# Optimization experiments

Measured on AMD Instinct MI355X. Metric: run time of the kernel, lower is better.

## Reference

```python
import jax, jax.numpy as jnp
import numpy as np
import math

D_IN = 1024
D_OUT = 1024
NUM_HEADS = 16
HEAD_DIM = D_OUT // NUM_HEADS
B = 2
S = 4096


def setup_inputs() -> dict:
    key = jax.random.key(0)
    ks = jax.random.split(key, 6)
    x = jax.random.normal(ks[0], (B, S, D_IN), dtype=jnp.float32)
    # kaiming-uniform-ish scale for weights; exact init values don't matter for correctness
    bound = 1.0 / math.sqrt(D_IN)
    Wq = jax.random.uniform(ks[1], (D_OUT, D_IN), minval=-bound, maxval=bound, dtype=jnp.float32)
    Wk = jax.random.uniform(ks[2], (D_OUT, D_IN), minval=-bound, maxval=bound, dtype=jnp.float32)
    Wv = jax.random.uniform(ks[3], (D_OUT, D_IN), minval=-bound, maxval=bound, dtype=jnp.float32)
    Wo = jax.random.uniform(ks[4], (D_OUT, D_OUT), minval=-bound, maxval=bound, dtype=jnp.float32)
    bo = jax.random.uniform(ks[5], (D_OUT,), minval=-bound, maxval=bound, dtype=jnp.float32)
    return {"x": x, "Wq": Wq, "Wk": Wk, "Wv": Wv, "Wo": Wo, "bo": bo}


@jax.custom_vjp
def binarize(w):
    return jnp.sign(w)

def _bin_fwd(w):
    return jnp.sign(w), w

def _bin_bwd(w, g):
    # straight-through estimator: pass grad where |w| <= 1
    return (g * (jnp.abs(w) <= 1).astype(g.dtype),)

binarize.defvjp(_bin_fwd, _bin_bwd)


def reference(x, Wq, Wk, Wv, Wo, bo):
    b, n, _ = x.shape
    h, hd = NUM_HEADS, HEAD_DIM
    # binarized projections (torch F.linear: x @ W.T)
    q = (x @ binarize(Wq).T).reshape(b, n, h, hd).transpose(0, 2, 1, 3)  # [b,h,n,hd]
    k = (x @ binarize(Wk).T).reshape(b, n, h, hd).transpose(0, 2, 1, 3)
    v = (x @ binarize(Wv).T).reshape(b, n, h, hd).transpose(0, 2, 1, 3)
    scores = jnp.einsum('bhqd,bhkd->bhqk', q, k) / math.sqrt(hd)  # [b,h,n,n]
    causal = jnp.tril(jnp.ones((n, n), dtype=bool))
    scores = jnp.where(causal, scores, -jnp.inf)
    attn = jax.nn.softmax(scores, axis=-1)
    # dropout p=0.0 -> identity
    ctx = jnp.einsum('bhqk,bhkd->bqhd', attn, v).reshape(b, n, h * hd)
    return ctx @ binarize(Wo).T + bo
```

## Files before the change

### kernel.cpp

```cpp
#include <hip/hip_runtime.h>
#include <hip/hip_bf16.h>
#include <cstdint>
#include <cstddef>

#define S 4096
#define D 1024
#define H 16
#define HD 64
#define BATCH 2
#define M_TOK 8192
#define K2 2048

typedef short short8 __attribute__((ext_vector_type(8)));
typedef __bf16 bf16x8 __attribute__((ext_vector_type(8)));
typedef float f32x4 __attribute__((ext_vector_type(4)));
typedef float f32x16 __attribute__((ext_vector_type(16)));
typedef unsigned int u32;

static __device__ __forceinline__ ushort f2bf(float f) {
  union { float f; uint32_t u; } v; v.f = f;
  uint32_t u = v.u + 0x7FFFu + ((v.u >> 16) & 1u);
  return (ushort)(u >> 16);
}
static __device__ __forceinline__ float bf2f(ushort h) {
  union { uint32_t u; float f; } v; v.u = ((uint32_t)h) << 16; return v.f;
}
static __device__ __forceinline__ uint32_t cvtpk(float lo, float hi) {
  uint32_t r;
  asm("v_cvt_pk_bf16_f32 %0, %1, %2" : "=v"(r) : "v"(lo), "v"(hi));
  return r;
}
static __device__ __forceinline__ float vexp2(float x) {
  float r;
  asm("v_exp_f32 %0, %1" : "=v"(r) : "v"(x));
  return r;
}
static __device__ __forceinline__ bf16x8 pack4(uint32_t a, uint32_t b, uint32_t c, uint32_t d) {
  union { uint32_t u[4]; bf16x8 v; } z;
  z.u[0] = a; z.u[1] = b; z.u[2] = c; z.u[3] = d;
  return z.v;
}
static __device__ __forceinline__ void gld16(const void* g, void* l) {
  __builtin_amdgcn_global_load_lds(
      (const __attribute__((address_space(1))) u32*)g,
      (__attribute__((address_space(3))) u32*)l, 16, 0, 0);
}
static __device__ __forceinline__ ushort sgn(float a) {
  return a > 0.f ? 0x3F80 : (a < 0.f ? 0xBF80 : 0);
}

__global__ void prep_x(const float* __restrict__ x, ushort* __restrict__ xcat) {
  int i = blockIdx.x * blockDim.x + threadIdx.x;
  const int total = M_TOK * 128;
  for (; i < total; i += gridDim.x * blockDim.x) {
    int row = i >> 7, c8 = (i & 127) * 8;
    const float* px = &x[(size_t)row * 1024 + c8];
    float4 a = *(const float4*)px;
    float4 b = *(const float4*)(px + 4);
    float va[8] = {a.x, a.y, a.z, a.w, b.x, b.y, b.z, b.w};
    union { ushort u[8]; short8 v; } Hh, Ll;
#pragma unroll
    for (int j = 0; j < 8; ++j) {
      ushort h = f2bf(va[j]);
      Hh.u[j] = h;
      Ll.u[j] = f2bf(va[j] - bf2f(h));
    }
    *(short8*)&xcat[(size_t)row * K2 + c8] = Hh.v;
    *(short8*)&xcat[(size_t)row * K2 + 1024 + c8] = Ll.v;
  }
}

__global__ void prep_w(const float* __restrict__ wq, const float* __restrict__ wk,
                       const float* __restrict__ wv, const float* __restrict__ wo,
                       ushort* __restrict__ wcat, ushort* __restrict__ wob) {
  int i = blockIdx.x * blockDim.x + threadIdx.x;
  const int total = (D * D) / 4;
  for (; i < total; i += gridDim.x * blockDim.x) {
    float4 a;
    union { ushort u[4]; uint2 v; } t;
    a = *(const float4*)&wq[i * 4];
    t.u[0] = sgn(a.x); t.u[1] = sgn(a.y); t.u[2] = sgn(a.z); t.u[3] = sgn(a.w);
    *(uint2*)&wcat[i * 4] = t.v;
    a = *(const float4*)&wk[i * 4];
    t.u[0] = sgn(a.x); t.u[1] = sgn(a.y); t.u[2] = sgn(a.z); t.u[3] = sgn(a.w);
    *(uint2*)&wcat[D * D + i * 4] = t.v;
    a = *(const float4*)&wv[i * 4];
    t.u[0] = sgn(a.x); t.u[1] = sgn(a.y); t.u[2] = sgn(a.z); t.u[3] = sgn(a.w);
    *(uint2*)&wcat[2 * D * D + i * 4] = t.v;
    a = *(const float4*)&wo[i * 4];
    t.u[0] = sgn(a.x); t.u[1] = sgn(a.y); t.u[2] = sgn(a.z); t.u[3] = sgn(a.w);
    *(uint2*)&wob[i * 4] = t.v;
  }
}

__global__ __launch_bounds__(512, 2) void gemm256(
    const ushort* __restrict__ A, const ushort* __restrict__ Bw,
    ushort* __restrict__ q_hi, ushort* __restrict__ q_lo,
    ushort* __restrict__ k_hi, ushort* __restrict__ k_lo)
{
  __shared__ ushort smA[3][256 * 32];
  __shared__ ushort smB[3][256 * 32];
  const int tid = threadIdx.x;
  const int l = tid & 63;
  const int w = tid >> 6;
  const int x = l & 15, g = l >> 4;
  const int wm = w >> 2, wn = w & 3;
  const int bm = blockIdx.x, bn = blockIdx.y;

  const ushort* gA[2]; const ushort* gB[2]; int ldso[2];
#pragma unroll
  for (int r = 0; r < 2; ++r) {
    int q = r * 512 + tid;
    int row = q >> 2;
    int blk = (q & 3) ^ ((row & 3) ^ ((row >> 2) & 3));
    gA[r] = &A[(size_t)(bm * 256 + row) * 2048 + blk * 8];
    gB[r] = &Bw[(size_t)(bn * 256 + row) * 1024 + blk * 8];
    ldso[r] = (r * 512 + w * 64) * 8;
  }

  f32x4 acc[8][4] = {};

#pragma unroll
  for (int r = 0; r < 2; ++r) {
    gld16(gA[r] + 0, &smA[0][ldso[r]]);
    gld16(gB[r] + 0, &smB[0][ldso[r]]);
  }
#pragma unroll
  for (int r = 0; r < 2; ++r) {
    gld16(gA[r] + 32, &smA[1][ldso[r]]);
    gld16(gB[r] + ((32) & 1023), &smB[1][ldso[r]]);
  }

  const int swz = (x & 3) ^ ((x >> 2) & 3);
  int cb = 0;
  for (int s = 0; s < 64; ++s) {
    if (s < 63) {
      asm volatile("s_waitcnt vmcnt(4)" ::: "memory");
    } else {
      asm volatile("s_waitcnt vmcnt(0)" ::: "memory");
    }
    __builtin_amdgcn_s_barrier();

    if (s + 2 < 64) {
      int nb = cb - 1; if (nb < 0) nb = 2;
      int k0 = (s + 2) * 32;
#pragma unroll
      for (int r = 0; r < 2; ++r) {
        gld16(gA[r] + k0, &smA[nb][ldso[r]]);
        gld16(gB[r] + (k0 & 1023), &smB[nb][ldso[r]]);
      }
    }

    const ushort* bA = smA[cb];
    const ushort* bB = smB[cb];
    bf16x8 af[8], bf_[4];
#pragma unroll
    for (int m = 0; m < 8; ++m)
      af[m] = *(const bf16x8*)&bA[(wm * 128 + m * 16 + x) * 32 + (g ^ swz) * 8];
#pragma unroll
    for (int n = 0; n < 4; ++n)
      bf_[n] = *(const bf16x8*)&bB[(wn * 64 + n * 16 + x) * 32 + (g ^ swz) * 8];

    __builtin_amdgcn_s_setprio(1);
#pragma unroll
    for (int m = 0; m < 8; ++m)
#pragma unroll
      for (int n = 0; n < 4; ++n)
        acc[m][n] = __builtin_amdgcn_mfma_f32_16x16x32_bf16(af[m], bf_[n], acc[m][n], 0, 0, 0);
    __builtin_amdgcn_s_setprio(0);

    cb = (cb == 2) ? 0 : cb + 1;
  }

#pragma unroll
  for (int m = 0; m < 8; ++m)
#pragma unroll
    for (int n = 0; n < 4; ++n)
#pragma unroll
      for (int r = 0; r < 4; ++r) {
        int rowg = bm * 256 + wm * 128 + m * 16 + g * 4 + r;
        int colg = bn * 256 + wn * 64 + n * 16 + x;
        float v = acc[m][n][r];
        int bi = rowg >> 12, ntok = rowg & 4095;
        int proj = colg >> 10;
        int cg = colg & 1023;
        int h = cg >> 6, hd = cg & 63;
        ushort* oh = (proj == 0) ? q_hi : k_hi;
        ushort* ol = (proj == 0) ? q_lo : k_lo;
        size_t off = (size_t)(bi * H + h) * (S * HD) + (size_t)ntok * HD + hd;
        ushort hiv = f2bf(v);
        oh[off] = hiv;
        ol[off] = f2bf(v - bf2f(hiv));
      }
}

template<int EPI, int KK, int BROW, int AST>
__global__ __launch_bounds__(256) void gemm97(
    const ushort* __restrict__ A, const ushort* __restrict__ Bw,
    ushort* __restrict__ v_t,
    float* __restrict__ of, const float* __restrict__ bias)
{
  __shared__ ushort smA[128 * 32];
  __shared__ ushort smB[128 * 32];
  const int tid = threadIdx.x;
  const int l = tid & 63;
  const int w = tid >> 6;
  const int x = l & 15, g = l >> 4;
  const int wm = w >> 1, wn = w & 1;
  const int bm = blockIdx.x, bn = blockIdx.y;

  const ushort* gA[2]; const ushort* gB[2]; int ldso[2];
#pragma unroll
  for (int p = 0; p < 2; ++p) {
    int q = p * 256 + tid;
    gA[p] = &A[(size_t)(bm * 128 + (q >> 2)) * AST + (q & 3) * 8];
    gB[p] = &Bw[(size_t)(bn * 128 + (q >> 2)) * BROW + (q & 3) * 8];
    ldso[p] = (p * 256 + w * 64) * 8;
  }

  f32x4 acc[4][4] = {};

  for (int k0 = 0; k0 < KK; k0 += 32) {
    __syncthreads();
#pragma unroll
    for (int p = 0; p < 2; ++p) {
      gld16(gA[p] + k0, &smA[ldso[p]]);
      gld16(gB[p] + (k0 & (BROW - 1)), &smB[ldso[p]]);
    }
    __syncthreads();
    bf16x8 af[4], bf_[4];
#pragma unroll
    for (int m = 0; m < 4; ++m)
      af[m] = *(const bf16x8*)&smA[(wm * 64 + m * 16 + x) * 32 + g * 8];
#pragma unroll
    for (int n = 0; n < 4; ++n)
      bf_[n] = *(const bf16x8*)&smB[(wn * 64 + n * 16 + x) * 32 + g * 8];
#pragma unroll
    for (int m = 0; m < 4; ++m)
#pragma unroll
      for (int n = 0; n < 4; ++n)
        acc[m][n] = __builtin_amdgcn_mfma_f32_16x16x32_bf16(af[m], bf_[n], acc[m][n], 0, 0, 0);
  }

#pragma unroll
  for (int m = 0; m < 4; ++m)
#pragma unroll
    for (int n = 0; n < 4; ++n)
#pragma unroll
      for (int r = 0; r < 4; ++r) {
        int rowg = bm * 128 + wm * 64 + m * 16 + g * 4 + r;
        int colg = bn * 128 + wn * 64 + n * 16 + x;
        float v = acc[m][n][r];
        if (EPI == 2) {
          of[(size_t)rowg * D + colg] = v + bias[colg];
        } else {
          int bi = rowg >> 12, ntok = rowg & 4095;
          int cg = colg & 1023;
          int h = cg >> 6, hd = cg & 63;
          size_t bhb = (size_t)(bi * H + h) * (S * HD);
          v_t[bhb + (size_t)hd * S + ntok] = f2bf(v);
        }
      }
}

__global__ __launch_bounds__(256) void flash16(
    const ushort* __restrict__ qhi, const ushort* __restrict__ qlo,
    const ushort* __restrict__ khi, const ushort* __restrict__ klo,
    const ushort* __restrict__ vt, ushort* __restrict__ ctx)
{
  __shared__ ushort smKhi[2][64 * 64];
  __shared__ ushort smKlo[2][64 * 64];
  __shared__ ushort smVT[2][64 * 64];

  const int tid = threadIdx.x;
  const int l = tid & 63;
  const int w = tid >> 6;
  const int q31 = l & 31;
  const int g2 = l >> 5;
  const int l7 = l & 7;
  const int bh = blockIdx.x;
  const int qt = (int)(gridDim.y - 1) - (int)blockIdx.y;
  const int qbase = qt * 128;
  const size_t qkbase = (size_t)bh * S * HD;

  int soff_k[2]; size_t soff_v[2]; int ldso[2];
#pragma unroll
  for (int p = 0; p < 2; ++p) {
    int q = p * 256 + tid;
    int r2 = q >> 3;
    int sb = (q & 7) ^ (r2 & 7);
    soff_k[p] = r2 * HD + sb * 8;
    soff_v[p] = (size_t)r2 * S + sb * 8;
    ldso[p] = (p * 256 + w * 64) * 8;
  }
  const ushort* khb = khi + qkbase;
  const ushort* klb = klo + qkbase;
  const ushort* vtb = vt + qkbase;

  bf16x8 bq[2][4];
  {
    int qrow = qbase + w * 32 + q31;
    size_t base = qkbase + (size_t)qrow * HD + g2 * 8;
#pragma unroll
    for (int s2 = 0; s2 < 4; ++s2) {
      bq[0][s2] = *(const bf16x8*)&qhi[base + s2 * 16];
      bq[1][s2] = *(const bf16x8*)&qlo[base + s2 * 16];
    }
  }

  float mrun = -1e30f;
  float lrun = 0.f;
  f32x16 oacc0 = {}, oacc1 = {};

  const int kvmax = (qbase + 127) >> 6;
  const int qmaxw = qbase + w * 32 + 31;
  const float C1 = 0.125f * 1.44269504f;
  const float TH = 8.0f / C1;

#pragma unroll
  for (int p = 0; p < 2; ++p) {
    gld16(khb + soff_k[p], &smKhi[0][ldso[p]]);
    gld16(klb + soff_k[p], &smKlo[0][ldso[p]]);
    gld16(vtb + soff_v[p], &smVT[0][ldso[p]]);
  }
  __syncthreads();

  int cur = 0;
  for (int kv = 0; kv <= kvmax; ++kv) {
    if (kv < kvmax) {
      const ushort* kh = khb + (size_t)(kv + 1) * (64 * HD);
      const ushort* kl = klb + (size_t)(kv + 1) * (64 * HD);
      const ushort* vp = vtb + (size_t)(kv + 1) * 64;
      int nb = cur ^ 1;
#pragma unroll
      for (int p = 0; p < 2; ++p) {
        gld16(kh + soff_k[p], &smKhi[nb][ldso[p]]);
        gld16(kl + soff_k[p], &smKlo[nb][ldso[p]]);
        gld16(vp + soff_v[p], &smVT[nb][ldso[p]]);
      }
    }

    if (kv * 64 <= qmaxw) {
      const ushort* bKhi = smKhi[cur];
      const ushort* bKlo = smKlo[cur];
      const ushort* bVT = smVT[cur];

      f32x16 sc0 = {}, sc1 = {};
      __builtin_amdgcn_s_setprio(1);
#pragma unroll
      for (int s2 = 0; s2 < 4; ++s2) {
        {
          int row = q31;
          int pb = row * 64 + (((2 * s2 + g2)) ^ l7) * 8;
          bf16x8 kH = *(const bf16x8*)&bKhi[pb];
          bf16x8 kL = *(const bf16x8*)&bKlo[pb];
          sc0 = __builtin_amdgcn_mfma_f32_32x32x16_bf16(kH, bq[0][s2], sc0, 0, 0, 0);
          sc0 = __builtin_amdgcn_mfma_f32_32x32x16_bf16(kL, bq[0][s2], sc0, 0, 0, 0);
          sc0 = __builtin_amdgcn_mfma_f32_32x32x16_bf16(kH, bq[1][s2], sc0, 0, 0, 0);
        }
        {
          int row = 32 + q31;
          int pb = row * 64 + (((2 * s2 + g2)) ^ l7) * 8;
          bf16x8 kH = *(const bf16x8*)&bKhi[pb];
          bf16x8 kL = *(const bf16x8*)&bKlo[pb];
          sc1 = __builtin_amdgcn_mfma_f32_32x32x16_bf16(kH, bq[0][s2], sc1, 0, 0, 0);
          sc1 = __builtin_amdgcn_mfma_f32_32x32x16_bf16(kL, bq[0][s2], sc1, 0, 0, 0);
          sc1 = __builtin_amdgcn_mfma_f32_32x32x16_bf16(kH, bq[1][s2], sc1, 0, 0, 0);
        }
      }
      __builtin_amdgcn_s_setprio(0);

      if (kv * 64 + 63 > qbase + w * 32) {
        int qglob = qbase + w * 32 + q31;
        int kb = kv * 64 + 4 * g2;
#pragma unroll
        for (int r = 0; r < 16; ++r) {
          int k5 = (r & 3) + 8 * (r >> 2);
          if (kb + k5 > qglob) sc0[r] = -1e30f;
          if (kb + 32 + k5 > qglob) sc1[r] = -1e30f;
        }
      }

      float mt[8];
#pragma unroll
      for (int r = 0; r < 8; ++r)
        mt[r] = fmaxf(fmaxf(sc0[2 * r], sc0[2 * r + 1]), fmaxf(sc1[2 * r], sc1[2 * r + 1]));
      float mloc = fmaxf(fmaxf(fmaxf(mt[0], mt[1]), fmaxf(mt[2], mt[3])),
                         fmaxf(fmaxf(mt[4], mt[5]), fmaxf(mt[6], mt[7])));
      if (__any(mloc > mrun + TH)) {
        float mx = fmaxf(mloc, __shfl_xor(mloc, 32));
        float mnew = fmaxf(mrun, mx);
        float scal = vexp2((mrun - mnew) * C1);
        mrun = mnew;
        lrun *= scal;
        oacc0 *= scal;
        oacc1 *= scal;
      }
      float mc = mrun * C1;
#pragma unroll
      for (int r = 0; r < 16; ++r) {
        sc0[r] = vexp2(sc0[r] * C1 - mc);
        sc1[r] = vexp2(sc1[r] * C1 - mc);
      }
      float st[8];
#pragma unroll
      for (int r = 0; r < 8; ++r)
        st[r] = (sc0[2 * r] + sc0[2 * r + 1]) + (sc1[2 * r] + sc1[2 * r + 1]);
      lrun += ((st[0] + st[1]) + (st[2] + st[3])) + ((st[4] + st[5]) + (st[6] + st[7]));

      uint32_t pbw[4][4];
#pragma unroll
      for (int s2 = 0; s2 < 4; ++s2) {
        const int s1 = s2 & 1;
#pragma unroll
        for (int p = 0; p < 2; ++p) {
          uint32_t a, b;
          if (s2 < 2) {
            a = cvtpk(sc0[2 * p + 8 * s1], sc0[2 * p + 1 + 8 * s1]);
            b = cvtpk(sc0[2 * p + 4 + 8 * s1], sc0[2 * p + 5 + 8 * s1]);
          } else {
            a = cvtpk(sc1[2 * p + 8 * s1], sc1[2 * p + 1 + 8 * s1]);
            b = cvtpk(sc1[2 * p + 4 + 8 * s1], sc1[2 * p + 5 + 8 * s1]);
          }
          asm volatile("v_permlane32_swap_b32 %0, %1" : "+v"(a), "+v"(b));
          pbw[s2][p] = a;
          pbw[s2][2 + p] = b;
        }
      }

      __builtin_amdgcn_s_setprio(1);
#pragma unroll
      for (int s2 = 0; s2 < 4; ++s2) {
        bf16x8 bp = pack4(pbw[s2][0], pbw[s2][1], pbw[s2][2], pbw[s2][3]);
        {
          bf16x8 vf = *(const bf16x8*)&bVT[(q31)*64 + (((2 * s2 + g2)) ^ l7) * 8];
          oacc0 = __builtin_amdgcn_mfma_f32_32x32x16_bf16(vf, bp, oacc0, 0, 0, 0);
        }
        {
          bf16x8 vf = *(const bf16x8*)&bVT[(32 + q31) * 64 + (((2 * s2 + g2)) ^ l7) * 8];
          oacc1 = __builtin_amdgcn_mfma_f32_32x32x16_bf16(vf, bp, oacc1, 0, 0, 0);
        }
      }
      __builtin_amdgcn_s_setprio(0);
    }

    __syncthreads();
    cur ^= 1;
  }

  const int b = bh >> 4, h = bh & 15;
  {
    float ls = lrun + __shfl_xor(lrun, 32);
    float inv = 1.0f / ls;
    int tok = qbase + w * 32 + q31;
    size_t rbase = (size_t)(b * S + tok) * D + h * 64;
#pragma unroll
    for (int r2 = 0; r2 < 4; ++r2) {
      uint2 uu;
      uu.x = cvtpk(oacc0[4 * r2] * inv, oacc0[4 * r2 + 1] * inv);
      uu.y = cvtpk(oacc0[4 * r2 + 2] * inv, oacc0[4 * r2 + 3] * inv);
      *(uint2*)&ctx[rbase + 8 * r2 + 4 * g2] = uu;
      uu.x = cvtpk(oacc1[4 * r2] * inv, oacc1[4 * r2 + 1] * inv);
      uu.y = cvtpk(oacc1[4 * r2 + 2] * inv, oacc1[4 * r2 + 3] * inv);
      *(uint2*)&ctx[rbase + 32 + 8 * r2 + 4 * g2] = uu;
    }
  }
}

extern "C" void kernel_launch(void* const* d_in, const int* in_sizes, int n_in,
                              void* d_out, int out_size, void* d_ws, size_t ws_size,
                              hipStream_t stream) {
  const float* x  = (const float*)d_in[0];
  const float* Wq = (const float*)d_in[1];
  const float* Wk = (const float*)d_in[2];
  const float* Wv = (const float*)d_in[3];
  const float* Wo = (const float*)d_in[4];
  const float* bo = (const float*)d_in[5];
  float* out = (float*)d_out;

  if (ws_size < (size_t)120 * 1024 * 1024) return;

  char* ws = (char*)d_ws;
  const size_t MB = 1024 * 1024;
  ushort* xcat = (ushort*)(ws);
  ushort* ctx  = (ushort*)(ws);
  ushort* wcat = (ushort*)(ws + 32 * MB);
  ushort* wob  = (ushort*)(ws + 38 * MB);
  ushort* qhi  = (ushort*)(ws + 40 * MB);
  ushort* qlo  = (ushort*)(ws + 56 * MB);
  ushort* khi  = (ushort*)(ws + 72 * MB);
  ushort* klo  = (ushort*)(ws + 88 * MB);
  ushort* vt   = (ushort*)(ws + 104 * MB);

  prep_x<<<2048, 256, 0, stream>>>(x, xcat);
  prep_w<<<1024, 256, 0, stream>>>(Wq, Wk, Wv, Wo, wcat, wob);

  gemm256<<<dim3(32, 8), 512, 0, stream>>>(xcat, wcat, qhi, qlo, khi, klo);
  gemm97<1, 1024, 1024, 2048><<<dim3(64, 8), 256, 0, stream>>>(
      xcat, wcat + 2 * D * D, vt, nullptr, nullptr);

  flash16<<<dim3(BATCH * H, S / 128), 256, 0, stream>>>(qhi, qlo, khi, klo, vt, ctx);

  gemm97<2, 1024, 1024, 1024><<<dim3(64, 8), 256, 0, stream>>>(
      ctx, wob, nullptr, out, bo);
}
```

Before: 321.0 us.

## Fold V projection into the QK projection GEMM launch with variable K-loop length

The V projection GEMM, previously its own launch, now runs as four extra column-tile groups of the big 256x256 QK GEMM grid. Those blocks run a shorter K loop (32 steps over the hi part only) and write bf16 V transposed. This removes one kernel launch and fills the device with more blocks in a single wave schedule. In exchange the grid becomes load-imbalanced because V blocks finish in half the time, and the epilogue now carries a branch.

```diff
diff --git a/kernel.cpp b/kernel.cpp
--- a/kernel.cpp
+++ b/kernel.cpp
@@ -96,7 +96,8 @@
 __global__ __launch_bounds__(512, 2) void gemm256(
     const ushort* __restrict__ A, const ushort* __restrict__ Bw,
     ushort* __restrict__ q_hi, ushort* __restrict__ q_lo,
-    ushort* __restrict__ k_hi, ushort* __restrict__ k_lo)
+    ushort* __restrict__ k_hi, ushort* __restrict__ k_lo,
+    ushort* __restrict__ v_t)
 {
   __shared__ ushort smA[3][256 * 32];
   __shared__ ushort smB[3][256 * 32];
@@ -106,6 +107,7 @@
   const int x = l & 15, g = l >> 4;
   const int wm = w >> 2, wn = w & 3;
   const int bm = blockIdx.x, bn = blockIdx.y;
+  const int NS = (bn < 8) ? 64 : 32;
 
   const ushort* gA[2]; const ushort* gB[2]; int ldso[2];
 #pragma unroll
@@ -133,15 +135,15 @@
 
   const int swz = (x & 3) ^ ((x >> 2) & 3);
   int cb = 0;
-  for (int s = 0; s < 64; ++s) {
-    if (s < 63) {
+  for (int s = 0; s < NS; ++s) {
+    if (s < NS - 1) {
       asm volatile("s_waitcnt vmcnt(4)" ::: "memory");
     } else {
       asm volatile("s_waitcnt vmcnt(0)" ::: "memory");
     }
     __builtin_amdgcn_s_barrier();
 
-    if (s + 2 < 64) {
+    if (s + 2 < NS) {
       int nb = cb - 1; if (nb < 0) nb = 2;
       int k0 = (s + 2) * 32;
 #pragma unroll
@@ -182,22 +184,26 @@
         int colg = bn * 256 + wn * 64 + n * 16 + x;
         float v = acc[m][n][r];
         int bi = rowg >> 12, ntok = rowg & 4095;
-        int proj = colg >> 10;
         int cg = colg & 1023;
         int h = cg >> 6, hd = cg & 63;
-        ushort* oh = (proj == 0) ? q_hi : k_hi;
-        ushort* ol = (proj == 0) ? q_lo : k_lo;
-        size_t off = (size_t)(bi * H + h) * (S * HD) + (size_t)ntok * HD + hd;
-        ushort hiv = f2bf(v);
-        oh[off] = hiv;
-        ol[off] = f2bf(v - bf2f(hiv));
-      }
-}
-
-template<int EPI, int KK, int BROW, int AST>
-__global__ __launch_bounds__(256) void gemm97(
+        size_t bhb = (size_t)(bi * H + h) * (S * HD);
+        if (bn < 8) {
+          int proj = colg >> 10;
+          ushort* oh = (proj == 0) ? q_hi : k_hi;
+          ushort* ol = (proj == 0) ? q_lo : k_lo;
+          size_t off = bhb + (size_t)ntok * HD + hd;
+          ushort hiv = f2bf(v);
+          oh[off] = hiv;
+          ol[off] = f2bf(v - bf2f(hiv));
+        } else {
+          v_t[bhb + (size_t)hd * S + ntok] = f2bf(v);
+        }
+      }
+}
+
+template<int KK, int BROW, int AST>
+__global__ __launch_bounds__(256) void gemm97o(
     const ushort* __restrict__ A, const ushort* __restrict__ Bw,
-    ushort* __restrict__ v_t,
     float* __restrict__ of, const float* __restrict__ bias)
 {
   __shared__ ushort smA[128 * 32];
@@ -250,16 +256,7 @@
       for (int r = 0; r < 4; ++r) {
         int rowg = bm * 128 + wm * 64 + m * 16 + g * 4 + r;
         int colg = bn * 128 + wn * 64 + n * 16 + x;
-        float v = acc[m][n][r];
-        if (EPI == 2) {
-          of[(size_t)rowg * D + colg] = v + bias[colg];
-        } else {
-          int bi = rowg >> 12, ntok = rowg & 4095;
-          int cg = colg & 1023;
-          int h = cg >> 6, hd = cg & 63;
-          size_t bhb = (size_t)(bi * H + h) * (S * HD);
-          v_t[bhb + (size_t)hd * S + ntok] = f2bf(v);
-        }
+        of[(size_t)rowg * D + colg] = acc[m][n][r] + bias[colg];
       }
 }
 
@@ -350,8 +347,7 @@
 #pragma unroll
       for (int s2 = 0; s2 < 4; ++s2) {
         {
-          int row = q31;
-          int pb = row * 64 + (((2 * s2 + g2)) ^ l7) * 8;
+          int pb = q31 * 64 + (((2 * s2 + g2)) ^ l7) * 8;
           bf16x8 kH = *(const bf16x8*)&bKhi[pb];
           bf16x8 kL = *(const bf16x8*)&bKlo[pb];
           sc0 = __builtin_amdgcn_mfma_f32_32x32x16_bf16(kH, bq[0][s2], sc0, 0, 0, 0);
@@ -359,8 +355,7 @@
           sc0 = __builtin_amdgcn_mfma_f32_32x32x16_bf16(kH, bq[1][s2], sc0, 0, 0, 0);
         }
         {
-          int row = 32 + q31;
-          int pb = row * 64 + (((2 * s2 + g2)) ^ l7) * 8;
+          int pb = (32 + q31) * 64 + (((2 * s2 + g2)) ^ l7) * 8;
           bf16x8 kH = *(const bf16x8*)&bKhi[pb];
           bf16x8 kL = *(const bf16x8*)&bKlo[pb];
           sc1 = __builtin_amdgcn_mfma_f32_32x32x16_bf16(kH, bq[0][s2], sc1, 0, 0, 0);
@@ -495,12 +490,9 @@
   prep_x<<<2048, 256, 0, stream>>>(x, xcat);
   prep_w<<<1024, 256, 0, stream>>>(Wq, Wk, Wv, Wo, wcat, wob);
 
-  gemm256<<<dim3(32, 8), 512, 0, stream>>>(xcat, wcat, qhi, qlo, khi, klo);
-  gemm97<1, 1024, 1024, 2048><<<dim3(64, 8), 256, 0, stream>>>(
-      xcat, wcat + 2 * D * D, vt, nullptr, nullptr);
+  gemm256<<<dim3(32, 12), 512, 0, stream>>>(xcat, wcat, qhi, qlo, khi, klo, vt);
 
   flash16<<<dim3(BATCH * H, S / 128), 256, 0, stream>>>(qhi, qlo, khi, klo, vt, ctx);
 
-  gemm97<2, 1024, 1024, 1024><<<dim3(64, 8), 256, 0, stream>>>(
-      ctx, wob, nullptr, out, bo);
-}
+  gemm97o<1024, 1024, 1024><<<dim3(64, 8), 256, 0, stream>>>(ctx, wob, out, bo);
+}
```

Result: slower. 358.0 us (+11.5%).

## Triple-buffer LDS in 128-tile GEMM with async prefetch and XOR swizzle

Applied to the files above, without the earlier changes.

Converts the 128x128 GEMM used for the V projection and output projection from a single-buffered load-sync-compute loop into a three-stage LDS ring. Loads for stage s+2 are issued while stage s is computed, with a partial vmcnt wait and a single barrier per step. Global-to-LDS placement and fragment reads get an XOR swizzle to reduce LDS bank conflicts, and MFMA issue priority is raised. This triples the LDS footprint per block, which may lower occupancy.

```diff
diff --git a/kernel.cpp b/kernel.cpp
--- a/kernel.cpp
+++ b/kernel.cpp
@@ -195,51 +195,84 @@
 }
 
 template<int EPI, int KK, int BROW, int AST>
-__global__ __launch_bounds__(256) void gemm97(
+__global__ __launch_bounds__(256) void gemm128p(
     const ushort* __restrict__ A, const ushort* __restrict__ Bw,
     ushort* __restrict__ v_t,
     float* __restrict__ of, const float* __restrict__ bias)
 {
-  __shared__ ushort smA[128 * 32];
-  __shared__ ushort smB[128 * 32];
+  __shared__ ushort smA[3][128 * 32];
+  __shared__ ushort smB[3][128 * 32];
   const int tid = threadIdx.x;
   const int l = tid & 63;
   const int w = tid >> 6;
   const int x = l & 15, g = l >> 4;
   const int wm = w >> 1, wn = w & 1;
   const int bm = blockIdx.x, bn = blockIdx.y;
+  const int NS = KK / 32;
 
   const ushort* gA[2]; const ushort* gB[2]; int ldso[2];
 #pragma unroll
-  for (int p = 0; p < 2; ++p) {
-    int q = p * 256 + tid;
-    gA[p] = &A[(size_t)(bm * 128 + (q >> 2)) * AST + (q & 3) * 8];
-    gB[p] = &Bw[(size_t)(bn * 128 + (q >> 2)) * BROW + (q & 3) * 8];
-    ldso[p] = (p * 256 + w * 64) * 8;
+  for (int r = 0; r < 2; ++r) {
+    int q = r * 256 + tid;
+    int row = q >> 2;
+    int blk = (q & 3) ^ ((row & 3) ^ ((row >> 2) & 3));
+    gA[r] = &A[(size_t)(bm * 128 + row) * AST + blk * 8];
+    gB[r] = &Bw[(size_t)(bn * 128 + row) * BROW + blk * 8];
+    ldso[r] = (r * 256 + w * 64) * 8;
   }
 
   f32x4 acc[4][4] = {};
 
-  for (int k0 = 0; k0 < KK; k0 += 32) {
-    __syncthreads();
-#pragma unroll
-    for (int p = 0; p < 2; ++p) {
-      gld16(gA[p] + k0, &smA[ldso[p]]);
-      gld16(gB[p] + (k0 & (BROW - 1)), &smB[ldso[p]]);
-    }
-    __syncthreads();
+#pragma unroll
+  for (int r = 0; r < 2; ++r) {
+    gld16(gA[r] + 0, &smA[0][ldso[r]]);
+    gld16(gB[r] + 0, &smB[0][ldso[r]]);
+  }
+#pragma unroll
+  for (int r = 0; r < 2; ++r) {
+    gld16(gA[r] + 32, &smA[1][ldso[r]]);
+    gld16(gB[r] + ((32) & (BROW - 1)), &smB[1][ldso[r]]);
+  }
+
+  const int swz = (x & 3) ^ ((x >> 2) & 3);
+  int cb = 0;
+  for (int s = 0; s < NS; ++s) {
+    if (s < NS - 1) {
+      asm volatile("s_waitcnt vmcnt(4)" ::: "memory");
+    } else {
+      asm volatile("s_waitcnt vmcnt(0)" ::: "memory");
+    }
+    __builtin_amdgcn_s_barrier();
+
+    if (s + 2 < NS) {
+      int nb = cb - 1; if (nb < 0) nb = 2;
+      int k0 = (s + 2) * 32;
+#pragma unroll
+      for (int r = 0; r < 2; ++r) {
+        gld16(gA[r] + k0, &smA[nb][ldso[r]]);
+        gld16(gB[r] + (k0 & (BROW - 1)), &smB[nb][ldso[r]]);
+      }
+    }
+
+    const ushort* bA = smA[cb];
+    const ushort* bB = smB[cb];
     bf16x8 af[4], bf_[4];
 #pragma unroll
     for (int m = 0; m < 4; ++m)
-      af[m] = *(const bf16x8*)&smA[(wm * 64 + m * 16 + x) * 32 + g * 8];
+      af[m] = *(const bf16x8*)&bA[(wm * 64 + m * 16 + x) * 32 + (g ^ swz) * 8];
 #pragma unroll
     for (int n = 0; n < 4; ++n)
-      bf_[n] = *(const bf16x8*)&smB[(wn * 64 + n * 16 + x) * 32 + g * 8];
+      bf_[n] = *(const bf16x8*)&bB[(wn * 64 + n * 16 + x) * 32 + (g ^ swz) * 8];
+
+    __builtin_amdgcn_s_setprio(1);
 #pragma unroll
     for (int m = 0; m < 4; ++m)
 #pragma unroll
       for (int n = 0; n < 4; ++n)
         acc[m][n] = __builtin_amdgcn_mfma_f32_16x16x32_bf16(af[m], bf_[n], acc[m][n], 0, 0, 0);
+    __builtin_amdgcn_s_setprio(0);
+
+    cb = (cb == 2) ? 0 : cb + 1;
   }
 
 #pragma unroll
@@ -350,8 +383,7 @@
 #pragma unroll
       for (int s2 = 0; s2 < 4; ++s2) {
         {
-          int row = q31;
-          int pb = row * 64 + (((2 * s2 + g2)) ^ l7) * 8;
+          int pb = q31 * 64 + (((2 * s2 + g2)) ^ l7) * 8;
           bf16x8 kH = *(const bf16x8*)&bKhi[pb];
           bf16x8 kL = *(const bf16x8*)&bKlo[pb];
           sc0 = __builtin_amdgcn_mfma_f32_32x32x16_bf16(kH, bq[0][s2], sc0, 0, 0, 0);
@@ -359,8 +391,7 @@
           sc0 = __builtin_amdgcn_mfma_f32_32x32x16_bf16(kH, bq[1][s2], sc0, 0, 0, 0);
         }
         {
-          int row = 32 + q31;
-          int pb = row * 64 + (((2 * s2 + g2)) ^ l7) * 8;
+          int pb = (32 + q31) * 64 + (((2 * s2 + g2)) ^ l7) * 8;
           bf16x8 kH = *(const bf16x8*)&bKhi[pb];
           bf16x8 kL = *(const bf16x8*)&bKlo[pb];
           sc1 = __builtin_amdgcn_mfma_f32_32x32x16_bf16(kH, bq[0][s2], sc1, 0, 0, 0);
@@ -496,11 +527,11 @@
   prep_w<<<1024, 256, 0, stream>>>(Wq, Wk, Wv, Wo, wcat, wob);
 
   gemm256<<<dim3(32, 8), 512, 0, stream>>>(xcat, wcat, qhi, qlo, khi, klo);
-  gemm97<1, 1024, 1024, 2048><<<dim3(64, 8), 256, 0, stream>>>(
+  gemm128p<1, 1024, 1024, 2048><<<dim3(64, 8), 256, 0, stream>>>(
       xcat, wcat + 2 * D * D, vt, nullptr, nullptr);
 
   flash16<<<dim3(BATCH * H, S / 128), 256, 0, stream>>>(qhi, qlo, khi, klo, vt, ctx);
 
-  gemm97<2, 1024, 1024, 1024><<<dim3(64, 8), 256, 0, stream>>>(
+  gemm128p<2, 1024, 1024, 1024><<<dim3(64, 8), 256, 0, stream>>>(
       ctx, wob, nullptr, out, bo);
 }
```

Result: slower. 327.9 us (+2.1%).
